# Performance work log

Hardware: AMD Instinct MI355X
Metric: run time of the kernel (lower is better)

The kernel has to match this reference:

```python
import jax, jax.numpy as jnp
import numpy as np

T, B, D, E, H = 64, 1024, 128, 256, 512


def _gru(x_emb, h0, W_ih, W_hh, b_ih, b_hh):
    """Standard GRU (PyTorch gate convention) over time-major x_emb [T,B,E]."""
    xW = x_emb @ W_ih + b_ih  # [T,B,3H], precompute input contractions

    def step(h, xw):
        hW = h @ W_hh + b_hh
        xr, xz, xn = jnp.split(xw, 3, axis=-1)
        hr, hz, hn = jnp.split(hW, 3, axis=-1)
        r = jax.nn.sigmoid(xr + hr)
        z = jax.nn.sigmoid(xz + hz)
        n = jnp.tanh(xn + r * hn)
        h_new = (1.0 - z) * n + z * h
        return h_new, h_new

    h_t, ys = jax.lax.scan(step, h0, xW)
    return ys, h_t


def setup_inputs() -> dict:
    key = jax.random.key(0)
    ks = jax.random.split(key, 16)
    s_in = 1.0 / np.sqrt(D)
    s_emb = 1.0 / np.sqrt(E)
    s_hid = 1.0 / np.sqrt(H)
    return {
        "past_input": jax.random.normal(ks[0], (T, B, D), jnp.float32),
        "future_input": jax.random.normal(ks[1], (T, B, D), jnp.float32),
        "noise": jax.random.normal(ks[2], (B, H), jnp.float32),
        "W_emb": jax.random.normal(ks[3], (D, E), jnp.float32) * s_in,
        "b_emb": jnp.zeros((E,), jnp.float32),
        "W_ih_enc": jax.random.normal(ks[4], (E, 3 * H), jnp.float32) * s_emb,
        "W_hh_enc": jax.random.normal(ks[5], (H, 3 * H), jnp.float32) * s_hid,
        "b_ih_enc": jnp.zeros((3 * H,), jnp.float32),
        "b_hh_enc": jnp.zeros((3 * H,), jnp.float32),
        "W_ih_dec": jax.random.normal(ks[6], (E, 3 * H), jnp.float32) * s_emb,
        "W_hh_dec": jax.random.normal(ks[7], (H, 3 * H), jnp.float32) * s_hid,
        "b_ih_dec": jnp.zeros((3 * H,), jnp.float32),
        "b_hh_dec": jnp.zeros((3 * H,), jnp.float32),
        "W_out": jax.random.normal(ks[8], (H, D), jnp.float32) * s_hid,
        "b_out": jnp.zeros((D,), jnp.float32),
    }


def reference(past_input, future_input, noise, W_emb, b_emb,
              W_ih_enc, W_hh_enc, b_ih_enc, b_hh_enc,
              W_ih_dec, W_hh_dec, b_ih_dec, b_hh_dec,
              W_out, b_out):
    past_emb = jax.nn.relu(past_input @ W_emb + b_emb)      # [T,B,E]
    fut_emb = jax.nn.relu(future_input @ W_emb + b_emb)     # [T,B,E]

    h0 = jnp.zeros((past_emb.shape[1], W_hh_enc.shape[0]), past_emb.dtype)
    _, h_t = _gru(past_emb, h0, W_ih_enc, W_hh_enc, b_ih_enc, b_hh_enc)

    # shift future embedding: step 0 -> zeros, step t -> emb at t-1
    fut_shift = jnp.concatenate([jnp.zeros_like(fut_emb[:1]), fut_emb[:-1]], axis=0)

    hidden = h_t + noise
    future_target, _ = _gru(fut_shift, hidden, W_ih_dec, W_hh_dec, b_ih_dec, b_hh_dec)
    return future_target @ W_out + b_out  # [T,B,D]
```

## Files before the change

kernel.cpp:

```cpp
#include <hip/hip_runtime.h>

typedef __bf16 bf16;
typedef __bf16 bf16x8 __attribute__((ext_vector_type(8)));
typedef float f32x4 __attribute__((ext_vector_type(4)));
typedef unsigned uint32x4 __attribute__((ext_vector_type(4)));

#define Tt 64
#define Bb 1024
#define Dd 128
#define Ee 256
#define Hh 512
#define H3 1536

__device__ __forceinline__ float sigmf(float x) { return 1.0f / (1.0f + __expf(-x)); }
__device__ __forceinline__ float tanhfast(float x) {
    float e = __expf(2.0f * x);
    return 1.0f - 2.0f / (e + 1.0f);
}

#define LD_SC(dst, bp, OFF) \
    asm volatile("global_load_dwordx4 %0, %1, off offset:" #OFF " sc1" : "=&v"(dst) : "v"(bp))
#define ST_SC(bp, OFF, val) \
    asm volatile("global_store_short %0, %1, off offset:" #OFF " sc1" :: "v"(bp), "v"(val))

__device__ __forceinline__ bool has_sent(bf16x8 v) {
    uint32x4 w = __builtin_bit_cast(uint32x4, v);
    bool m = false;
#pragma unroll
    for (int i = 0; i < 4; ++i) {
        m = m || ((w[i] & 0xFFFFu) == 0xFFFFu) || ((w[i] >> 16) == 0xFFFFu);
    }
    return m;
}

__global__ void k_prep(const float* __restrict__ We, const float* __restrict__ Wie, const float* __restrict__ Whe,
                       const float* __restrict__ Wid, const float* __restrict__ Whd, const float* __restrict__ Wo,
                       bf16* __restrict__ dWe, bf16* __restrict__ dWie, bf16* __restrict__ dWhe,
                       bf16* __restrict__ dWid, bf16* __restrict__ dWhd, bf16* __restrict__ dWo) {
    long i = (long)blockIdx.x * 256 + threadIdx.x;
    const float* s;
    bf16* d;
    int K, N;
    if (i < 32768) { s = We; d = dWe; K = Dd; N = Ee; }
    else if ((i -= 32768) < 393216) { s = Wie; d = dWie; K = Ee; N = H3; }
    else if ((i -= 393216) < 786432) { s = Whe; d = dWhe; K = Hh; N = H3; }
    else if ((i -= 786432) < 393216) { s = Wid; d = dWid; K = Ee; N = H3; }
    else if ((i -= 393216) < 786432) { s = Whd; d = dWhd; K = Hh; N = H3; }
    else if ((i -= 786432) < 65536) { s = Wo; d = dWo; K = Hh; N = Dd; }
    else return;
    int n = (int)(i / K), k = (int)(i - (long)n * K);
    d[i] = (bf16)s[(size_t)k * N + n];
}

__global__ __launch_bounds__(256) void k_embed(const float* __restrict__ xP, const float* __restrict__ xF,
                                               const bf16* __restrict__ WT, const float* __restrict__ bias,
                                               bf16* __restrict__ oP, bf16* __restrict__ oF) {
    const int lane = threadIdx.x & 63, wv = threadIdx.x >> 6;
    const float* x = blockIdx.z ? xF : xP;
    bf16* o = blockIdx.z ? oF : oP;
    const int m0w = blockIdx.x * 128 + wv * 32;
    const int c0 = blockIdx.y * 64;
    const int koff = (lane >> 4) * 8;
    f32x4 acc[2][4];
#pragma unroll
    for (int m = 0; m < 2; ++m)
#pragma unroll
        for (int s = 0; s < 4; ++s) acc[m][s] = f32x4{0.f, 0.f, 0.f, 0.f};

    const float* xp0 = x + (size_t)(m0w + (lane & 15)) * Dd + koff;
#pragma unroll
    for (int kc = 0; kc < 4; ++kc) {
        bf16x8 a0, a1;
        {
            float4 f0 = *(const float4*)(xp0 + kc * 32);
            float4 f1 = *(const float4*)(xp0 + kc * 32 + 4);
            a0[0] = (bf16)f0.x; a0[1] = (bf16)f0.y; a0[2] = (bf16)f0.z; a0[3] = (bf16)f0.w;
            a0[4] = (bf16)f1.x; a0[5] = (bf16)f1.y; a0[6] = (bf16)f1.z; a0[7] = (bf16)f1.w;
            float4 g0 = *(const float4*)(xp0 + 16 * Dd + kc * 32);
            float4 g1 = *(const float4*)(xp0 + 16 * Dd + kc * 32 + 4);
            a1[0] = (bf16)g0.x; a1[1] = (bf16)g0.y; a1[2] = (bf16)g0.z; a1[3] = (bf16)g0.w;
            a1[4] = (bf16)g1.x; a1[5] = (bf16)g1.y; a1[6] = (bf16)g1.z; a1[7] = (bf16)g1.w;
        }
#pragma unroll
        for (int s = 0; s < 4; ++s) {
            bf16x8 b = *(const bf16x8*)(WT + (size_t)(c0 + s * 16 + (lane & 15)) * Dd + kc * 32 + koff);
            acc[0][s] = __builtin_amdgcn_mfma_f32_16x16x32_bf16(a0, b, acc[0][s], 0, 0, 0);
            acc[1][s] = __builtin_amdgcn_mfma_f32_16x16x32_bf16(a1, b, acc[1][s], 0, 0, 0);
        }
    }
#pragma unroll
    for (int m = 0; m < 2; ++m)
#pragma unroll
        for (int s = 0; s < 4; ++s) {
            int col = c0 + s * 16 + (lane & 15);
            float bv = bias[col];
#pragma unroll
            for (int r = 0; r < 4; ++r) {
                int row = m0w + m * 16 + (lane >> 4) * 4 + r;
                o[(size_t)row * Ee + col] = (bf16)fmaxf(acc[m][s][r] + bv, 0.0f);
            }
        }
}

__global__ __launch_bounds__(256, 1) void k_gru_all(
    const bf16* __restrict__ embP, const bf16* __restrict__ embF, const float* __restrict__ noise,
    const bf16* __restrict__ WihE, const bf16* __restrict__ WhhE,
    const float* __restrict__ bIhE, const float* __restrict__ bHhE,
    const bf16* __restrict__ WihD, const bf16* __restrict__ WhhD,
    const float* __restrict__ bIhD, const float* __restrict__ bHhD,
    bf16* __restrict__ henc, bf16* __restrict__ hmid, bf16* __restrict__ ys) {
    __shared__ bf16 Wih[6 * 8 * 64 * 8];
    __shared__ bf16 Whh[6 * 16 * 64 * 8];
    const int tid = threadIdx.x;
    const int lane = tid & 63, rh = tid >> 6;
    const int bid = blockIdx.x;
    const int im = (bid & 7) * 2 + (bid >> 7);
    const int in = (bid >> 3) & 15;
    const int rowb = im * 64 + rh * 16;
    const int arow0 = rowb + (lane & 15);
    const int koff = (lane >> 4) * 8;
    const int colc0 = in * 32 + (lane & 15);

    const bf16x8* WihV = (const bf16x8*)Wih;
    const bf16x8* WhhV = (const bf16x8*)Whh;

    auto stage = [&](const bf16* WT, int Kdim, int KC, bf16* lds) {
        int total = 6 * KC * 64;
        for (int idx = tid; idx < total; idx += 256) {
            int ln = idx & 63;
            int kc = (idx >> 6) % KC;
            int s = (idx >> 6) / KC;
            int gate = s >> 1, f = s & 1;
            int col = gate * Hh + in * 32 + f * 16 + (ln & 15);
            int k = kc * 32 + (ln >> 4) * 8;
            *(bf16x8*)(lds + (size_t)idx * 8) = *(const bf16x8*)(WT + (size_t)col * Kdim + k);
        }
    };

    float bi[3][2], bh[3][2];
    auto load_bias = [&](const float* bIh, const float* bHh) {
#pragma unroll
        for (int g = 0; g < 3; ++g)
#pragma unroll
            for (int f = 0; f < 2; ++f) {
                int c = g * Hh + colc0 + f * 16;
                bi[g][f] = bIh[c];
                bh[g][f] = bHh[c];
            }
    };

    f32x4 aR[2], aZ[2], aNX[2], aNH[2];
    auto zacc = [&]() {
#pragma unroll
        for (int f = 0; f < 2; ++f) {
            aR[f] = f32x4{0.f, 0.f, 0.f, 0.f};
            aZ[f] = f32x4{0.f, 0.f, 0.f, 0.f};
            aNX[f] = f32x4{0.f, 0.f, 0.f, 0.f};
            aNH[f] = f32x4{0.f, 0.f, 0.f, 0.f};
        }
    };

    auto xp_phase = [&](const bf16* xp) {
        const bf16* ap = xp + (size_t)arow0 * Ee + koff;
#pragma unroll
        for (int kc = 0; kc < 8; ++kc) {
            bf16x8 a = *(const bf16x8*)(ap + kc * 32);
#pragma unroll
            for (int f = 0; f < 2; ++f) {
                aR[f] = __builtin_amdgcn_mfma_f32_16x16x32_bf16(a, WihV[((0 + f) * 8 + kc) * 64 + lane], aR[f], 0, 0, 0);
                aZ[f] = __builtin_amdgcn_mfma_f32_16x16x32_bf16(a, WihV[((2 + f) * 8 + kc) * 64 + lane], aZ[f], 0, 0, 0);
                aNX[f] = __builtin_amdgcn_mfma_f32_16x16x32_bf16(a, WihV[((4 + f) * 8 + kc) * 64 + lane], aNX[f], 0, 0, 0);
            }
        }
    };

    auto hw_phase = [&](const bf16* hp) {
        const bf16* h0p = hp + (size_t)arow0 * Hh + koff;
        bf16x8 h0[16];
        LD_SC(h0[0], h0p, 0);    LD_SC(h0[1], h0p, 64);   LD_SC(h0[2], h0p, 128);  LD_SC(h0[3], h0p, 192);
        LD_SC(h0[4], h0p, 256);  LD_SC(h0[5], h0p, 320);  LD_SC(h0[6], h0p, 384);  LD_SC(h0[7], h0p, 448);
        LD_SC(h0[8], h0p, 512);  LD_SC(h0[9], h0p, 576);  LD_SC(h0[10], h0p, 640); LD_SC(h0[11], h0p, 704);
        LD_SC(h0[12], h0p, 768); LD_SC(h0[13], h0p, 832); LD_SC(h0[14], h0p, 896); LD_SC(h0[15], h0p, 960);
        asm volatile("s_waitcnt vmcnt(0)" ::: "memory");
        unsigned fail = 0;
#define CK0(p) fail |= ((unsigned)__any((int)has_sent(h0[p]))) << p;
        CK0(0) CK0(1) CK0(2) CK0(3) CK0(4) CK0(5) CK0(6) CK0(7)
        CK0(8) CK0(9) CK0(10) CK0(11) CK0(12) CK0(13) CK0(14) CK0(15)
#undef CK0
#pragma unroll 1
        while (fail) {
            __builtin_amdgcn_s_sleep(1);
#define RT(p, OFF) if (fail & (1u << p)) { LD_SC(h0[p], h0p, OFF); }
            RT(0, 0)    RT(1, 64)   RT(2, 128)  RT(3, 192)
            RT(4, 256)  RT(5, 320)  RT(6, 384)  RT(7, 448)
            RT(8, 512)  RT(9, 576)  RT(10, 640) RT(11, 704)
            RT(12, 768) RT(13, 832) RT(14, 896) RT(15, 960)
#undef RT
            asm volatile("s_waitcnt vmcnt(0)" ::: "memory");
            unsigned nf = 0;
#define CK(p) if (fail & (1u << p)) { nf |= ((unsigned)__any((int)has_sent(h0[p]))) << p; }
            CK(0) CK(1) CK(2) CK(3) CK(4) CK(5) CK(6) CK(7)
            CK(8) CK(9) CK(10) CK(11) CK(12) CK(13) CK(14) CK(15)
#undef CK
            fail = nf;
        }
        __builtin_amdgcn_sched_barrier(0);
#pragma unroll
        for (int kc = 0; kc < 16; ++kc) {
#pragma unroll
            for (int f = 0; f < 2; ++f) {
                aR[f] = __builtin_amdgcn_mfma_f32_16x16x32_bf16(h0[kc], WhhV[((0 + f) * 16 + kc) * 64 + lane], aR[f], 0, 0, 0);
                aZ[f] = __builtin_amdgcn_mfma_f32_16x16x32_bf16(h0[kc], WhhV[((2 + f) * 16 + kc) * 64 + lane], aZ[f], 0, 0, 0);
                aNH[f] = __builtin_amdgcn_mfma_f32_16x16x32_bf16(h0[kc], WhhV[((4 + f) * 16 + kc) * 64 + lane], aNH[f], 0, 0, 0);
            }
        }
    };

    float hreg[8];
#pragma unroll
    for (int i = 0; i < 8; ++i) hreg[i] = 0.0f;

    auto epi = [&](bf16* op) {
#pragma unroll
        for (int f = 0; f < 2; ++f) {
            bf16* stb = op + (size_t)(rowb + (lane >> 4) * 4) * Hh + colc0 + f * 16;
            unsigned short us[4];
#pragma unroll
            for (int r = 0; r < 4; ++r) {
                float rg = sigmf(aR[f][r] + bi[0][f] + bh[0][f]);
                float zg = sigmf(aZ[f][r] + bi[1][f] + bh[1][f]);
                float ng = tanhfast(aNX[f][r] + bi[2][f] + rg * (aNH[f][r] + bh[2][f]));
                float hv = (1.0f - zg) * ng + zg * hreg[f * 4 + r];
                hreg[f * 4 + r] = hv;
                us[r] = __builtin_bit_cast(unsigned short, (bf16)hv);
            }
            ST_SC(stb, 0, us[0]);
            ST_SC(stb, 1024, us[1]);
            ST_SC(stb, 2048, us[2]);
            ST_SC(stb, 3072, us[3]);
        }
    };

    stage(WihE, Ee, 8, Wih);
    stage(WhhE, Hh, 16, Whh);
    load_bias(bIhE, bHhE);
    __syncthreads();

#pragma unroll 1
    for (int t = 0; t < Tt; ++t) {
        zacc();
        xp_phase(embP + (size_t)t * Bb * Ee);
        if (t > 0) hw_phase(henc + (size_t)(t - 1) * Bb * Hh);
        epi(henc + (size_t)t * Bb * Hh);
    }

    {
#pragma unroll
        for (int f = 0; f < 2; ++f) {
            bf16* stb = hmid + (size_t)(rowb + (lane >> 4) * 4) * Hh + colc0 + f * 16;
            unsigned short us[4];
#pragma unroll
            for (int r = 0; r < 4; ++r) {
                int row = rowb + (lane >> 4) * 4 + r;
                float v = hreg[f * 4 + r] + noise[(size_t)row * Hh + colc0 + f * 16];
                hreg[f * 4 + r] = v;
                us[r] = __builtin_bit_cast(unsigned short, (bf16)v);
            }
            ST_SC(stb, 0, us[0]);
            ST_SC(stb, 1024, us[1]);
            ST_SC(stb, 2048, us[2]);
            ST_SC(stb, 3072, us[3]);
        }
    }
    __syncthreads();
    stage(WihD, Ee, 8, Wih);
    stage(WhhD, Hh, 16, Whh);
    __syncthreads();
    load_bias(bIhD, bHhD);

#pragma unroll 1
    for (int t = 0; t < Tt; ++t) {
        zacc();
        if (t > 0) xp_phase(embF + (size_t)(t - 1) * Bb * Ee);
        hw_phase(t ? ys + (size_t)(t - 1) * Bb * Hh : hmid);
        epi(ys + (size_t)t * Bb * Hh);
    }
}

__global__ __launch_bounds__(256) void k_out(const bf16* __restrict__ ys, const bf16* __restrict__ WT,
                                             const float* __restrict__ bias, float* __restrict__ out) {
    const int lane = threadIdx.x & 63, wv = threadIdx.x >> 6;
    const int m0w = blockIdx.x * 256 + wv * 64;
    const int c0 = blockIdx.y * 64;
    const int koff = (lane >> 4) * 8;
    f32x4 acc[4][4];
#pragma unroll
    for (int m = 0; m < 4; ++m)
#pragma unroll
        for (int s = 0; s < 4; ++s) acc[m][s] = f32x4{0.f, 0.f, 0.f, 0.f};

    const bf16* ap = ys + (size_t)(m0w + (lane & 15)) * Hh + koff;
#pragma unroll
    for (int kc = 0; kc < 16; ++kc) {
        bf16x8 a0 = *(const bf16x8*)(ap + kc * 32);
        bf16x8 a1 = *(const bf16x8*)(ap + 16 * Hh + kc * 32);
        bf16x8 a2 = *(const bf16x8*)(ap + 32 * Hh + kc * 32);
        bf16x8 a3 = *(const bf16x8*)(ap + 48 * Hh + kc * 32);
#pragma unroll
        for (int s = 0; s < 4; ++s) {
            bf16x8 b = *(const bf16x8*)(WT + (size_t)(c0 + s * 16 + (lane & 15)) * Hh + kc * 32 + koff);
            acc[0][s] = __builtin_amdgcn_mfma_f32_16x16x32_bf16(a0, b, acc[0][s], 0, 0, 0);
            acc[1][s] = __builtin_amdgcn_mfma_f32_16x16x32_bf16(a1, b, acc[1][s], 0, 0, 0);
            acc[2][s] = __builtin_amdgcn_mfma_f32_16x16x32_bf16(a2, b, acc[2][s], 0, 0, 0);
            acc[3][s] = __builtin_amdgcn_mfma_f32_16x16x32_bf16(a3, b, acc[3][s], 0, 0, 0);
        }
    }
#pragma unroll
    for (int m = 0; m < 4; ++m)
#pragma unroll
        for (int s = 0; s < 4; ++s) {
            int col = c0 + s * 16 + (lane & 15);
            float bv = bias[col];
#pragma unroll
            for (int r = 0; r < 4; ++r) {
                int row = m0w + m * 16 + (lane >> 4) * 4 + r;
                out[(size_t)row * Dd + col] = acc[m][s][r] + bv;
            }
        }
}

extern "C" void kernel_launch(void* const* d_in, const int* in_sizes, int n_in,
                              void* d_out, int out_size, void* d_ws, size_t ws_size,
                              hipStream_t stream) {
    const float* past = (const float*)d_in[0];
    const float* fut = (const float*)d_in[1];
    const float* noise = (const float*)d_in[2];
    const float* W_emb = (const float*)d_in[3];
    const float* b_emb = (const float*)d_in[4];
    const float* W_ih_enc = (const float*)d_in[5];
    const float* W_hh_enc = (const float*)d_in[6];
    const float* b_ih_enc = (const float*)d_in[7];
    const float* b_hh_enc = (const float*)d_in[8];
    const float* W_ih_dec = (const float*)d_in[9];
    const float* W_hh_dec = (const float*)d_in[10];
    const float* b_ih_dec = (const float*)d_in[11];
    const float* b_hh_dec = (const float*)d_in[12];
    const float* W_out = (const float*)d_in[13];
    const float* b_out = (const float*)d_in[14];
    float* out = (float*)d_out;

    char* w = (char*)d_ws;
    auto alloc = [&](size_t bytes) {
        char* p = w;
        w += (bytes + 255) & ~(size_t)255;
        return p;
    };
    bf16* embP = (bf16*)alloc((size_t)Tt * Bb * Ee * 2);
    bf16* embF = (bf16*)alloc((size_t)Tt * Bb * Ee * 2);
    bf16* ys = (bf16*)alloc((size_t)Tt * Bb * Hh * 2);
    bf16* henc = (bf16*)alloc((size_t)Tt * Bb * Hh * 2);
    bf16* hmid = (bf16*)alloc((size_t)Bb * Hh * 2);
    bf16* WembT = (bf16*)alloc((size_t)Ee * Dd * 2);
    bf16* WihEncT = (bf16*)alloc((size_t)H3 * Ee * 2);
    bf16* WhhEncT = (bf16*)alloc((size_t)H3 * Hh * 2);
    bf16* WihDecT = (bf16*)alloc((size_t)H3 * Ee * 2);
    bf16* WhhDecT = (bf16*)alloc((size_t)H3 * Hh * 2);
    bf16* WoutT = (bf16*)alloc((size_t)Dd * Hh * 2);

    k_prep<<<9600, 256, 0, stream>>>(W_emb, W_ih_enc, W_hh_enc, W_ih_dec, W_hh_dec, W_out,
                                     WembT, WihEncT, WhhEncT, WihDecT, WhhDecT, WoutT);

    k_embed<<<dim3(Tt * Bb / 128, Ee / 64, 2), 256, 0, stream>>>(past, fut, WembT, b_emb, embP, embF);

    hipMemsetAsync(ys, 0xFF, (size_t)Tt * Bb * Hh * 2, stream);
    hipMemsetAsync(henc, 0xFF, (size_t)Tt * Bb * Hh * 2, stream);
    hipMemsetAsync(hmid, 0xFF, (size_t)Bb * Hh * 2, stream);

    void* args[] = {(void*)&embP, (void*)&embF, (void*)&noise,
                    (void*)&WihEncT, (void*)&WhhEncT, (void*)&b_ih_enc, (void*)&b_hh_enc,
                    (void*)&WihDecT, (void*)&WhhDecT, (void*)&b_ih_dec, (void*)&b_hh_dec,
                    (void*)&henc, (void*)&hmid, (void*)&ys};
    hipLaunchCooperativeKernel((const void*)k_gru_all, dim3(256), dim3(256), args, 0, stream);

    k_out<<<dim3(Tt * Bb / 256, Dd / 64), 256, 0, stream>>>(ys, WoutT, b_out, out);
}
```

Before: 1.160 ms.

## Add per-producer readiness flags to gate hidden-state loads in GRU

Adds a flag array where each producing wave writes a step sequence number after its epilogue. Consumers poll the flags of the 16 producers of their row band and issue each hidden-state chunk load only once that producer has signalled. The goal is to avoid repeatedly reloading whole vectors and retrying when sentinel values are still present. The cost is an extra flag store per step and polling loads with a waitcnt, which may add latency on the critical recurrent path. The sentinel check is kept as a fallback.

```diff
diff --git a/kernel.cpp b/kernel.cpp
--- a/kernel.cpp
+++ b/kernel.cpp
@@ -108,7 +108,7 @@
     const float* __restrict__ bIhE, const float* __restrict__ bHhE,
     const bf16* __restrict__ WihD, const bf16* __restrict__ WhhD,
     const float* __restrict__ bIhD, const float* __restrict__ bHhD,
-    bf16* __restrict__ henc, bf16* __restrict__ hmid, bf16* __restrict__ ys) {
+    bf16* __restrict__ henc, bf16* __restrict__ hmid, bf16* __restrict__ ys, unsigned* __restrict__ flags) {
     __shared__ bf16 Wih[6 * 8 * 64 * 8];
     __shared__ bf16 Whh[6 * 16 * 64 * 8];
     const int tid = threadIdx.x;
@@ -120,6 +120,7 @@
     const int arow0 = rowb + (lane & 15);
     const int koff = (lane >> 4) * 8;
     const int colc0 = in * 32 + (lane & 15);
+    unsigned* dom = flags + ((size_t)im * 4 + rh) * 16 * 16;
 
     const bf16x8* WihV = (const bf16x8*)Wih;
     const bf16x8* WhhV = (const bf16x8*)Whh;
@@ -149,6 +150,20 @@
             }
     };
 
+    auto signal = [&](unsigned seq) {
+        if (lane == 0) {
+            unsigned* fp = dom + in * 16;
+            asm volatile("global_store_dword %0, %1, off sc1" :: "v"(fp), "v"(seq) : "memory");
+        }
+    };
+    auto poll = [&](unsigned seq) -> unsigned long long {
+        unsigned v;
+        const unsigned* fp = dom + (lane & 15) * 16;
+        asm volatile("global_load_dword %0, %1, off sc1\n\ts_waitcnt vmcnt(0)"
+                     : "=&v"(v) : "v"(fp) : "memory");
+        return __ballot((int)(v >= seq));
+    };
+
     f32x4 aR[2], aZ[2], aNX[2], aNH[2];
     auto zacc = [&]() {
 #pragma unroll
@@ -174,13 +189,18 @@
         }
     };
 
-    auto hw_phase = [&](const bf16* hp) {
+    auto hw_phase = [&](const bf16* hp, unsigned seq) {
         const bf16* h0p = hp + (size_t)arow0 * Hh + koff;
         bf16x8 h0[16];
-        LD_SC(h0[0], h0p, 0);    LD_SC(h0[1], h0p, 64);   LD_SC(h0[2], h0p, 128);  LD_SC(h0[3], h0p, 192);
-        LD_SC(h0[4], h0p, 256);  LD_SC(h0[5], h0p, 320);  LD_SC(h0[6], h0p, 384);  LD_SC(h0[7], h0p, 448);
-        LD_SC(h0[8], h0p, 512);  LD_SC(h0[9], h0p, 576);  LD_SC(h0[10], h0p, 640); LD_SC(h0[11], h0p, 704);
-        LD_SC(h0[12], h0p, 768); LD_SC(h0[13], h0p, 832); LD_SC(h0[14], h0p, 896); LD_SC(h0[15], h0p, 960);
+        unsigned long long rdy = poll(seq);
+#define HSTEP(p, OFF) \
+        while (!((rdy >> p) & 1ULL)) { __builtin_amdgcn_s_sleep(1); rdy = poll(seq); } \
+        LD_SC(h0[p], h0p, OFF);
+        HSTEP(0, 0)    HSTEP(1, 64)   HSTEP(2, 128)  HSTEP(3, 192)
+        HSTEP(4, 256)  HSTEP(5, 320)  HSTEP(6, 384)  HSTEP(7, 448)
+        HSTEP(8, 512)  HSTEP(9, 576)  HSTEP(10, 640) HSTEP(11, 704)
+        HSTEP(12, 768) HSTEP(13, 832) HSTEP(14, 896) HSTEP(15, 960)
+#undef HSTEP
         asm volatile("s_waitcnt vmcnt(0)" ::: "memory");
         unsigned fail = 0;
 #define CK0(p) fail |= ((unsigned)__any((int)has_sent(h0[p]))) << p;
@@ -250,8 +270,9 @@
     for (int t = 0; t < Tt; ++t) {
         zacc();
         xp_phase(embP + (size_t)t * Bb * Ee);
-        if (t > 0) hw_phase(henc + (size_t)(t - 1) * Bb * Hh);
+        if (t > 0) hw_phase(henc + (size_t)(t - 1) * Bb * Hh, (unsigned)t);
         epi(henc + (size_t)t * Bb * Hh);
+        signal((unsigned)(t + 1));
     }
 
     {
@@ -277,13 +298,15 @@
     stage(WhhD, Hh, 16, Whh);
     __syncthreads();
     load_bias(bIhD, bHhD);
+    signal((unsigned)(Tt + 1));
 
 #pragma unroll 1
     for (int t = 0; t < Tt; ++t) {
         zacc();
         if (t > 0) xp_phase(embF + (size_t)(t - 1) * Bb * Ee);
-        hw_phase(t ? ys + (size_t)(t - 1) * Bb * Hh : hmid);
+        hw_phase(t ? ys + (size_t)(t - 1) * Bb * Hh : hmid, (unsigned)(Tt + 1 + t));
         epi(ys + (size_t)t * Bb * Hh);
+        if (t < Tt - 1) signal((unsigned)(Tt + 2 + t));
     }
 }
 
@@ -366,6 +389,7 @@
     bf16* WihDecT = (bf16*)alloc((size_t)H3 * Ee * 2);
     bf16* WhhDecT = (bf16*)alloc((size_t)H3 * Hh * 2);
     bf16* WoutT = (bf16*)alloc((size_t)Dd * Hh * 2);
+    unsigned* flags = (unsigned*)alloc(16 * 4 * 16 * 16 * sizeof(unsigned));
 
     k_prep<<<9600, 256, 0, stream>>>(W_emb, W_ih_enc, W_hh_enc, W_ih_dec, W_hh_dec, W_out,
                                      WembT, WihEncT, WhhEncT, WihDecT, WhhDecT, WoutT);
@@ -375,11 +399,12 @@
     hipMemsetAsync(ys, 0xFF, (size_t)Tt * Bb * Hh * 2, stream);
     hipMemsetAsync(henc, 0xFF, (size_t)Tt * Bb * Hh * 2, stream);
     hipMemsetAsync(hmid, 0xFF, (size_t)Bb * Hh * 2, stream);
+    hipMemsetAsync(flags, 0, 16 * 4 * 16 * 16 * sizeof(unsigned), stream);
 
     void* args[] = {(void*)&embP, (void*)&embF, (void*)&noise,
                     (void*)&WihEncT, (void*)&WhhEncT, (void*)&b_ih_enc, (void*)&b_hh_enc,
                     (void*)&WihDecT, (void*)&WhhDecT, (void*)&b_ih_dec, (void*)&b_hh_dec,
-                    (void*)&henc, (void*)&hmid, (void*)&ys};
+                    (void*)&henc, (void*)&hmid, (void*)&ys, (void*)&flags};
     hipLaunchCooperativeKernel((const void*)k_gru_all, dim3(256), dim3(256), args, 0, stream);
 
     k_out<<<dim3(Tt * Bb / 256, Dd / 64), 256, 0, stream>>>(ys, WoutT, b_out, out);
```

New measurement: 1.116 ms. 1.04x faster.
